# Optimization experiments

Measured on AMD Instinct MI355X. Metric: run time of the kernel, lower is better.

Reference implementation:

```python
import jax, jax.numpy as jnp
import numpy as np

# FP4 e2m1 lookup: nibble -> value (bit3 = sign, bits2:0 = e2m1 magnitude)
FP4_LUT = jnp.array([0.0, 0.5, 1.0, 1.5, 2.0, 3.0, 4.0, 6.0,
                     -0.0, -0.5, -1.0, -1.5, -2.0, -3.0, -4.0, -6.0], dtype=jnp.float32)
BLOCK = 16  # elements per micro-scale (one uint8 E8M0 scale per 16 fp4 values)


def _dequant(packed, sf):
    """packed: [R, K//2] int bytes (two fp4 nibbles each, low nibble first).
    sf: [R, K//16] E8M0 exponents (value = 2^(sf-127)). Returns [R, K] f32."""
    R, Kh = packed.shape
    K = Kh * 2
    lo = packed & 0xF
    hi = (packed >> 4) & 0xF
    nib = jnp.stack([lo, hi], axis=-1).reshape(R, K)
    vals = FP4_LUT[nib]  # [R, K]
    block_scale = jnp.exp2((sf - 127).astype(jnp.float32))  # [R, K//16]
    return (vals.reshape(R, K // BLOCK, BLOCK) * block_scale[:, :, None]).reshape(R, K)


def setup_inputs() -> dict:
    key = jax.random.key(0)
    ks = jax.random.split(key, 6)
    M, N, K = 8192, 4096, 4224  # K = in_features(4096) + select_num(128)
    A_packed = jax.random.randint(ks[0], (M, K // 2), 0, 256, dtype=jnp.int32)
    SFA = jax.random.randint(ks[1], (M, K // BLOCK), 118, 134, dtype=jnp.int32)
    B_packed = jax.random.randint(ks[2], (N, K // 2), 0, 256, dtype=jnp.int32)
    SFB = jax.random.randint(ks[3], (N, K // BLOCK), 118, 134, dtype=jnp.int32)
    scale = jax.random.uniform(ks[4], (1,), dtype=jnp.float32, minval=0.5, maxval=1.5)
    bias = jax.random.normal(ks[5], (N,), dtype=jnp.float32)
    return {"A_packed": A_packed, "SFA": SFA, "scale": scale,
            "B_packed": B_packed, "SFB": SFB, "bias": bias}


def reference(A_packed, SFA, scale, B_packed, SFB, bias):
    A = _dequant(A_packed, SFA)        # [M, K]
    B = _dequant(B_packed, SFB)        # [N, K]
    # y = scale * (A @ B^T) + bias   (self.scale == 1.0 folded into scale)
    y = scale[0] * jnp.einsum('mk,nk->mn', A, B) + bias[None, :]
    return y
```

## Files before the change

### kernel.cpp

```cpp
#include <hip/hip_runtime.h>
#include <stdint.h>

#define M_DIM 8192
#define N_DIM 4096
#define K_DIM 4224
#define BK 64

typedef float f32x16 __attribute__((ext_vector_type(16)));
typedef int   i32x8  __attribute__((ext_vector_type(8)));
typedef int   i32x4  __attribute__((ext_vector_type(4)));

#define RAW_BARRIER()  asm volatile("s_barrier" ::: "memory")
#define WAIT_VM4()     asm volatile("s_waitcnt vmcnt(4)" ::: "memory")
#define WAIT_VM0()     asm volatile("s_waitcnt vmcnt(0)" ::: "memory")

__device__ __forceinline__ uint32_t conv4(uint32_t x, uint32_t k1) {
    uint32_t n7   = x & 0x07070707u;
    uint32_t base = __builtin_amdgcn_perm(0x46444240u, 0x3E3C3800u, n7);
    uint32_t nz   = __builtin_amdgcn_perm(0x01010101u, 0x01010100u, n7);
    uint32_t sign = (x & 0x08080808u) << 4;
    return (base + nz * k1 - (nz << 6)) | sign;
}

__global__ __launch_bounds__(256) void dequant_all(
    const int* __restrict__ Ap, const int* __restrict__ SFA, uint8_t* __restrict__ Aout,
    const int* __restrict__ Bp, const int* __restrict__ SFB, uint8_t* __restrict__ Bout)
{
    const int nhA = M_DIM * K_DIM / 32;
    int i = blockIdx.x * 256 + threadIdx.x;
    const int* p; const int* sf; uint8_t* out; int idx;
    if (i < nhA) { p = Ap; sf = SFA; out = Aout; idx = i; }
    else         { p = Bp; sf = SFB; out = Bout; idx = i - nhA; }

    const int4* p4 = (const int4*)p;
    int4 q0 = p4[4 * idx];
    int4 q1 = p4[4 * idx + 1];
    int4 q2 = p4[4 * idx + 2];
    int4 q3 = p4[4 * idx + 3];
    int2 sfp = ((const int2*)sf)[idx];
    uint32_t k1a = (uint32_t)(((sfp.x - 127) << 2) + 64);
    uint32_t k1b = (uint32_t)(((sfp.y - 127) << 2) + 64);

    uint32_t o[8];
#pragma unroll
    for (int g = 0; g < 4; ++g) {
        int4 pg = (g == 0) ? q0 : (g == 1) ? q1 : (g == 2) ? q2 : q3;
        uint32_t k1 = (g < 2) ? k1a : k1b;
        uint32_t w = (uint32_t)(pg.x & 0xFF) | ((uint32_t)(pg.y & 0xFF) << 8) |
                     ((uint32_t)(pg.z & 0xFF) << 16) | ((uint32_t)pg.w << 24);
        uint32_t lr = conv4(w & 0x0F0F0F0Fu, k1);
        uint32_t hr = conv4((w >> 4) & 0x0F0F0F0Fu, k1);
        o[2 * g]     = __builtin_amdgcn_perm(hr, lr, 0x05010400u);
        o[2 * g + 1] = __builtin_amdgcn_perm(hr, lr, 0x07030602u);
    }
    *(uint4*)(out + (size_t)idx * 32)      = make_uint4(o[0], o[1], o[2], o[3]);
    *(uint4*)(out + (size_t)idx * 32 + 16) = make_uint4(o[4], o[5], o[6], o[7]);
}

__global__ __launch_bounds__(512, 2) void gemm_mx(
    const uint8_t* __restrict__ A, const uint8_t* __restrict__ B,
    const float* __restrict__ scale, const float* __restrict__ bias,
    float* __restrict__ C)
{
    __shared__ uint8_t smem[131072];

    const int tid  = threadIdx.x;
    const int lane = tid & 63;
    const int w    = tid >> 6;
    const int wm   = w >> 2;
    const int wn   = w & 3;
    const int r31  = lane & 31;
    const int h    = lane >> 5;

    const int lin = blockIdx.y * 16 + blockIdx.x;
    const int o   = (lin & 7) * 64 + (lin >> 3);
    const int bn0 = (o & 15) * 256;
    const int bm0 = (o >> 4) * 256;

    f32x16 acc[4][2];
#pragma unroll
    for (int i = 0; i < 4; ++i)
#pragma unroll
        for (int j = 0; j < 2; ++j)
            acc[i][j] = (f32x16)(0.0f);

    const int srow = lane >> 2;
    const int scol = (((lane & 3) ^ ((lane >> 3) & 3)) << 4);
    const uint8_t* Ag = A + (size_t)(bm0 + w * 32 + srow) * K_DIM + scol;
    const uint8_t* Bg = B + (size_t)(bn0 + w * 32 + srow) * K_DIM + scol;
    uint8_t* Asw = smem + w * 2048;
    uint8_t* Bsw = smem + 16384 + w * 2048;

#define STAGE(koff, boff)                                                        \
    do {                                                                         \
        const uint8_t* ag_ = Ag + (koff);                                        \
        const uint8_t* bg_ = Bg + (koff);                                        \
        __builtin_amdgcn_global_load_lds(                                        \
            (const __attribute__((address_space(1))) void*)(ag_),                \
            (__attribute__((address_space(3))) void*)(Asw + (boff)), 16, 0, 0);  \
        __builtin_amdgcn_global_load_lds(                                        \
            (const __attribute__((address_space(1))) void*)(ag_ + (size_t)16 * K_DIM), \
            (__attribute__((address_space(3))) void*)(Asw + (boff) + 1024), 16, 0, 0); \
        __builtin_amdgcn_global_load_lds(                                        \
            (const __attribute__((address_space(1))) void*)(bg_),                \
            (__attribute__((address_space(3))) void*)(Bsw + (boff)), 16, 0, 0);  \
        __builtin_amdgcn_global_load_lds(                                        \
            (const __attribute__((address_space(1))) void*)(bg_ + (size_t)16 * K_DIM), \
            (__attribute__((address_space(3))) void*)(Bsw + (boff) + 1024), 16, 0, 0); \
    } while (0)

    const int sx = (r31 >> 1) & 3;
    const uint8_t* pa_lo[4]; const uint8_t* pa_hi[4];
    const uint8_t* pb_lo[2]; const uint8_t* pb_hi[2];
#pragma unroll
    for (int mi = 0; mi < 4; ++mi) {
        const uint8_t* base = smem + (wm * 128 + mi * 32 + r31) * 64;
        pa_lo[mi] = base + (((2 * h)     ^ sx) << 4);
        pa_hi[mi] = base + (((2 * h + 1) ^ sx) << 4);
    }
#pragma unroll
    for (int ni = 0; ni < 2; ++ni) {
        const uint8_t* base = smem + 16384 + (wn * 64 + ni * 32 + r31) * 64;
        pb_lo[ni] = base + (((2 * h)     ^ sx) << 4);
        pb_hi[ni] = base + (((2 * h + 1) ^ sx) << 4);
    }

    i32x8 afX0[2], afX1[2], bfX0[2], bfX1[2], afY[2];

    auto rd = [&](const uint8_t* plo, const uint8_t* phi, int off, i32x8& dst) {
        i32x4 lo = *(const i32x4*)(plo + off);
        i32x4 hi = *(const i32x4*)(phi + off);
        dst = __builtin_shufflevector(lo, hi, 0, 1, 2, 3, 4, 5, 6, 7);
    };
    auto mm = [&](const i32x8& a, const i32x8& b, f32x16& c) {
        c = __builtin_amdgcn_mfma_scale_f32_32x32x64_f8f6f4(
                a, b, c, 1, 1, 0, 0x7F7F7F7F, 0, 0x7F7F7F7F);
    };

#define CORE(AC, BC, AN, BN, OBN)                             \
    __builtin_amdgcn_s_setprio(1);                            \
    mm(AC[0], BC[0], acc[0][0]); mm(AC[0], BC[1], acc[0][1]); \
    mm(AC[1], BC[0], acc[1][0]); mm(AC[1], BC[1], acc[1][1]); \
    __builtin_amdgcn_s_setprio(0);                            \
    rd(pa_lo[0], pa_hi[0], OBN, AN[0]);                       \
    rd(pa_lo[1], pa_hi[1], OBN, AN[1]);                       \
    rd(pb_lo[0], pb_hi[0], OBN, BN[0]);                       \
    rd(pb_lo[1], pb_hi[1], OBN, BN[1]);                       \
    __builtin_amdgcn_s_setprio(1);                            \
    mm(afY[0], BC[0], acc[2][0]); mm(afY[0], BC[1], acc[2][1]); \
    mm(afY[1], BC[0], acc[3][0]); mm(afY[1], BC[1], acc[3][1]); \
    __builtin_amdgcn_s_setprio(0);                            \
    rd(pa_lo[2], pa_hi[2], OBN, afY[0]);                      \
    rd(pa_lo[3], pa_hi[3], OBN, afY[1]);

#define BODY(T, AC, BC, AN, BN, OBN, OBS)                     \
    STAGE(((T) + 3) * BK, OBS);                               \
    CORE(AC, BC, AN, BN, OBN)                                 \
    WAIT_VM4(); RAW_BARRIER();

    STAGE(0 * BK, 0);
    STAGE(1 * BK, 32768);
    STAGE(2 * BK, 65536);
    WAIT_VM4();
    RAW_BARRIER();
    rd(pa_lo[0], pa_hi[0], 0, afX0[0]);
    rd(pa_lo[1], pa_hi[1], 0, afX0[1]);
    rd(pb_lo[0], pb_hi[0], 0, bfX0[0]);
    rd(pb_lo[1], pb_hi[1], 0, bfX0[1]);
    rd(pa_lo[2], pa_hi[2], 0, afY[0]);
    rd(pa_lo[3], pa_hi[3], 0, afY[1]);

#pragma unroll 1
    for (int g = 0; g < 15; ++g) {
        const int t = 4 * g;
        BODY(t,     afX0, bfX0, afX1, bfX1, 32768, 98304)
        BODY(t + 1, afX1, bfX1, afX0, bfX0, 65536, 0)
        BODY(t + 2, afX0, bfX0, afX1, bfX1, 98304, 32768)
        BODY(t + 3, afX1, bfX1, afX0, bfX0, 0,     65536)
    }
    BODY(60, afX0, bfX0, afX1, bfX1, 32768, 98304)
    BODY(61, afX1, bfX1, afX0, bfX0, 65536, 0)
    BODY(62, afX0, bfX0, afX1, bfX1, 98304, 32768)
    CORE(afX1, bfX1, afX0, bfX0, 0)
    WAIT_VM0(); RAW_BARRIER();
    CORE(afX0, bfX0, afX1, bfX1, 32768)
    __builtin_amdgcn_s_setprio(1);
    mm(afX1[0], bfX1[0], acc[0][0]); mm(afX1[0], bfX1[1], acc[0][1]);
    mm(afX1[1], bfX1[0], acc[1][0]); mm(afX1[1], bfX1[1], acc[1][1]);
    mm(afY[0],  bfX1[0], acc[2][0]); mm(afY[0],  bfX1[1], acc[2][1]);
    mm(afY[1],  bfX1[0], acc[3][0]); mm(afY[1],  bfX1[1], acc[3][1]);
    __builtin_amdgcn_s_setprio(0);
#undef BODY
#undef CORE
#undef STAGE

    const float sc = scale[0];
#pragma unroll
    for (int ni = 0; ni < 2; ++ni) {
        const int col = bn0 + wn * 64 + ni * 32 + r31;
        const float bv = bias[col];
#pragma unroll
        for (int mi = 0; mi < 4; ++mi) {
            const int rbase = bm0 + wm * 128 + mi * 32 + 4 * h;
#pragma unroll
            for (int reg = 0; reg < 16; ++reg) {
                const int row = rbase + (reg & 3) + 8 * (reg >> 2);
                C[(size_t)row * N_DIM + col] = sc * acc[mi][ni][reg] + bv;
            }
        }
    }
}

extern "C" void kernel_launch(void* const* d_in, const int* in_sizes, int n_in,
                              void* d_out, int out_size, void* d_ws, size_t ws_size,
                              hipStream_t stream) {
    const int*   A_packed = (const int*)d_in[0];
    const int*   SFA      = (const int*)d_in[1];
    const float* scale    = (const float*)d_in[2];
    const int*   B_packed = (const int*)d_in[3];
    const int*   SFB      = (const int*)d_in[4];
    const float* bias     = (const float*)d_in[5];
    float*       out      = (float*)d_out;

    uint8_t* Abf8 = (uint8_t*)d_ws;
    uint8_t* Bbf8 = Abf8 + (size_t)M_DIM * K_DIM;

    const int npairA = M_DIM * K_DIM / 32;
    const int npairB = N_DIM * K_DIM / 32;
    dequant_all<<<(npairA + npairB) / 256, 256, 0, stream>>>(
        A_packed, SFA, Abf8, B_packed, SFB, Bbf8);

    dim3 grid(N_DIM / 256, M_DIM / 256);
    gemm_mx<<<grid, 512, 0, stream>>>(Abf8, Bbf8, scale, bias, out);
}
```

Before: 340.4 us.

## Use 4 waves per block with 128x128 warp tiles in MX GEMM

Halves the threads per block from 512 to 256. Each wave now computes a 128x128 output tile (4x4 MFMA accumulators) instead of 128x64, so fragment reuse per LDS read goes up and per-wave LDS traffic per MFMA goes down. Each wave now issues 8 global-to-LDS loads per stage, and the wait count is raised to match. The cost is much higher register pressure (256 accumulator VGPRs plus doubled fragments) and fewer waves per CU to hide latency, with occupancy limited to one block.

```diff
diff --git a/kernel.cpp b/kernel.cpp
--- a/kernel.cpp
+++ b/kernel.cpp
@@ -11,7 +11,7 @@
 typedef int   i32x4  __attribute__((ext_vector_type(4)));
 
 #define RAW_BARRIER()  asm volatile("s_barrier" ::: "memory")
-#define WAIT_VM4()     asm volatile("s_waitcnt vmcnt(4)" ::: "memory")
+#define WAIT_VM8()     asm volatile("s_waitcnt vmcnt(8)" ::: "memory")
 #define WAIT_VM0()     asm volatile("s_waitcnt vmcnt(0)" ::: "memory")
 
 __device__ __forceinline__ uint32_t conv4(uint32_t x, uint32_t k1) {
@@ -57,7 +57,7 @@
     *(uint4*)(out + (size_t)idx * 32 + 16) = make_uint4(o[4], o[5], o[6], o[7]);
 }
 
-__global__ __launch_bounds__(512, 2) void gemm_mx(
+__global__ __launch_bounds__(256, 1) void gemm_mx(
     const uint8_t* __restrict__ A, const uint8_t* __restrict__ B,
     const float* __restrict__ scale, const float* __restrict__ bias,
     float* __restrict__ C)
@@ -67,8 +67,8 @@
     const int tid  = threadIdx.x;
     const int lane = tid & 63;
     const int w    = tid >> 6;
-    const int wm   = w >> 2;
-    const int wn   = w & 3;
+    const int wm   = w >> 1;
+    const int wn   = w & 1;
     const int r31  = lane & 31;
     const int h    = lane >> 5;
 
@@ -77,41 +77,42 @@
     const int bn0 = (o & 15) * 256;
     const int bm0 = (o >> 4) * 256;
 
-    f32x16 acc[4][2];
+    f32x16 acc[4][4];
 #pragma unroll
     for (int i = 0; i < 4; ++i)
 #pragma unroll
-        for (int j = 0; j < 2; ++j)
+        for (int j = 0; j < 4; ++j)
             acc[i][j] = (f32x16)(0.0f);
 
     const int srow = lane >> 2;
     const int scol = (((lane & 3) ^ ((lane >> 3) & 3)) << 4);
-    const uint8_t* Ag = A + (size_t)(bm0 + w * 32 + srow) * K_DIM + scol;
-    const uint8_t* Bg = B + (size_t)(bn0 + w * 32 + srow) * K_DIM + scol;
-    uint8_t* Asw = smem + w * 2048;
-    uint8_t* Bsw = smem + 16384 + w * 2048;
+    const uint8_t* Ag = A + (size_t)(bm0 + w * 64 + srow) * K_DIM + scol;
+    const uint8_t* Bg = B + (size_t)(bn0 + w * 64 + srow) * K_DIM + scol;
+    uint8_t* Asw = smem + w * 4096;
+    uint8_t* Bsw = smem + 16384 + w * 4096;
+
+#define GLDS(gp, lp)                                                             \
+    __builtin_amdgcn_global_load_lds(                                            \
+        (const __attribute__((address_space(1))) void*)(gp),                     \
+        (__attribute__((address_space(3))) void*)(lp), 16, 0, 0)
 
 #define STAGE(koff, boff)                                                        \
     do {                                                                         \
         const uint8_t* ag_ = Ag + (koff);                                        \
         const uint8_t* bg_ = Bg + (koff);                                        \
-        __builtin_amdgcn_global_load_lds(                                        \
-            (const __attribute__((address_space(1))) void*)(ag_),                \
-            (__attribute__((address_space(3))) void*)(Asw + (boff)), 16, 0, 0);  \
-        __builtin_amdgcn_global_load_lds(                                        \
-            (const __attribute__((address_space(1))) void*)(ag_ + (size_t)16 * K_DIM), \
-            (__attribute__((address_space(3))) void*)(Asw + (boff) + 1024), 16, 0, 0); \
-        __builtin_amdgcn_global_load_lds(                                        \
-            (const __attribute__((address_space(1))) void*)(bg_),                \
-            (__attribute__((address_space(3))) void*)(Bsw + (boff)), 16, 0, 0);  \
-        __builtin_amdgcn_global_load_lds(                                        \
-            (const __attribute__((address_space(1))) void*)(bg_ + (size_t)16 * K_DIM), \
-            (__attribute__((address_space(3))) void*)(Bsw + (boff) + 1024), 16, 0, 0); \
+        GLDS(ag_,                       Asw + (boff));                           \
+        GLDS(ag_ + (size_t)16 * K_DIM,  Asw + (boff) + 1024);                    \
+        GLDS(ag_ + (size_t)32 * K_DIM,  Asw + (boff) + 2048);                    \
+        GLDS(ag_ + (size_t)48 * K_DIM,  Asw + (boff) + 3072);                    \
+        GLDS(bg_,                       Bsw + (boff));                           \
+        GLDS(bg_ + (size_t)16 * K_DIM,  Bsw + (boff) + 1024);                    \
+        GLDS(bg_ + (size_t)32 * K_DIM,  Bsw + (boff) + 2048);                    \
+        GLDS(bg_ + (size_t)48 * K_DIM,  Bsw + (boff) + 3072);                    \
     } while (0)
 
     const int sx = (r31 >> 1) & 3;
     const uint8_t* pa_lo[4]; const uint8_t* pa_hi[4];
-    const uint8_t* pb_lo[2]; const uint8_t* pb_hi[2];
+    const uint8_t* pb_lo[4]; const uint8_t* pb_hi[4];
 #pragma unroll
     for (int mi = 0; mi < 4; ++mi) {
         const uint8_t* base = smem + (wm * 128 + mi * 32 + r31) * 64;
@@ -119,13 +120,13 @@
         pa_hi[mi] = base + (((2 * h + 1) ^ sx) << 4);
     }
 #pragma unroll
-    for (int ni = 0; ni < 2; ++ni) {
-        const uint8_t* base = smem + 16384 + (wn * 64 + ni * 32 + r31) * 64;
+    for (int ni = 0; ni < 4; ++ni) {
+        const uint8_t* base = smem + 16384 + (wn * 128 + ni * 32 + r31) * 64;
         pb_lo[ni] = base + (((2 * h)     ^ sx) << 4);
         pb_hi[ni] = base + (((2 * h + 1) ^ sx) << 4);
     }
 
-    i32x8 afX0[2], afX1[2], bfX0[2], bfX1[2], afY[2];
+    i32x8 afX0[4], afX1[4], bfX0[4], bfX1[4];
 
     auto rd = [&](const uint8_t* plo, const uint8_t* phi, int off, i32x8& dst) {
         i32x4 lo = *(const i32x4*)(plo + off);
@@ -137,46 +138,51 @@
                 a, b, c, 1, 1, 0, 0x7F7F7F7F, 0, 0x7F7F7F7F);
     };
 
+#define CLUSTER(AC, BC, MI)                                   \
+    __builtin_amdgcn_s_setprio(1);                            \
+    mm(AC[MI], BC[0], acc[MI][0]); mm(AC[MI], BC[1], acc[MI][1]); \
+    mm(AC[MI], BC[2], acc[MI][2]); mm(AC[MI], BC[3], acc[MI][3]); \
+    __builtin_amdgcn_s_setprio(0);
+
 #define CORE(AC, BC, AN, BN, OBN)                             \
-    __builtin_amdgcn_s_setprio(1);                            \
-    mm(AC[0], BC[0], acc[0][0]); mm(AC[0], BC[1], acc[0][1]); \
-    mm(AC[1], BC[0], acc[1][0]); mm(AC[1], BC[1], acc[1][1]); \
-    __builtin_amdgcn_s_setprio(0);                            \
+    CLUSTER(AC, BC, 0)                                        \
     rd(pa_lo[0], pa_hi[0], OBN, AN[0]);                       \
+    rd(pb_lo[0], pb_hi[0], OBN, BN[0]);                       \
+    CLUSTER(AC, BC, 1)                                        \
     rd(pa_lo[1], pa_hi[1], OBN, AN[1]);                       \
-    rd(pb_lo[0], pb_hi[0], OBN, BN[0]);                       \
     rd(pb_lo[1], pb_hi[1], OBN, BN[1]);                       \
-    __builtin_amdgcn_s_setprio(1);                            \
-    mm(afY[0], BC[0], acc[2][0]); mm(afY[0], BC[1], acc[2][1]); \
-    mm(afY[1], BC[0], acc[3][0]); mm(afY[1], BC[1], acc[3][1]); \
-    __builtin_amdgcn_s_setprio(0);                            \
-    rd(pa_lo[2], pa_hi[2], OBN, afY[0]);                      \
-    rd(pa_lo[3], pa_hi[3], OBN, afY[1]);
+    CLUSTER(AC, BC, 2)                                        \
+    rd(pa_lo[2], pa_hi[2], OBN, AN[2]);                       \
+    rd(pb_lo[2], pb_hi[2], OBN, BN[2]);                       \
+    CLUSTER(AC, BC, 3)                                        \
+    rd(pa_lo[3], pa_hi[3], OBN, AN[3]);                       \
+    rd(pb_lo[3], pb_hi[3], OBN, BN[3]);
 
 #define BODY(T, AC, BC, AN, BN, OBN, OBS)                     \
     STAGE(((T) + 3) * BK, OBS);                               \
     CORE(AC, BC, AN, BN, OBN)                                 \
-    WAIT_VM4(); RAW_BARRIER();
+    WAIT_VM8(); RAW_BARRIER();
 
     STAGE(0 * BK, 0);
     STAGE(1 * BK, 32768);
     STAGE(2 * BK, 65536);
-    WAIT_VM4();
+    WAIT_VM8();
     RAW_BARRIER();
     rd(pa_lo[0], pa_hi[0], 0, afX0[0]);
     rd(pa_lo[1], pa_hi[1], 0, afX0[1]);
+    rd(pa_lo[2], pa_hi[2], 0, afX0[2]);
+    rd(pa_lo[3], pa_hi[3], 0, afX0[3]);
     rd(pb_lo[0], pb_hi[0], 0, bfX0[0]);
     rd(pb_lo[1], pb_hi[1], 0, bfX0[1]);
-    rd(pa_lo[2], pa_hi[2], 0, afY[0]);
-    rd(pa_lo[3], pa_hi[3], 0, afY[1]);
+    rd(pb_lo[2], pb_hi[2], 0, bfX0[2]);
+    rd(pb_lo[3], pb_hi[3], 0, bfX0[3]);
 
 #pragma unroll 1
     for (int g = 0; g < 15; ++g) {
-        const int t = 4 * g;
-        BODY(t,     afX0, bfX0, afX1, bfX1, 32768, 98304)
-        BODY(t + 1, afX1, bfX1, afX0, bfX0, 65536, 0)
-        BODY(t + 2, afX0, bfX0, afX1, bfX1, 98304, 32768)
-        BODY(t + 3, afX1, bfX1, afX0, bfX0, 0,     65536)
+        BODY(4 * g,     afX0, bfX0, afX1, bfX1, 32768, 98304)
+        BODY(4 * g + 1, afX1, bfX1, afX0, bfX0, 65536, 0)
+        BODY(4 * g + 2, afX0, bfX0, afX1, bfX1, 98304, 32768)
+        BODY(4 * g + 3, afX1, bfX1, afX0, bfX0, 0,     65536)
     }
     BODY(60, afX0, bfX0, afX1, bfX1, 32768, 98304)
     BODY(61, afX1, bfX1, afX0, bfX0, 65536, 0)
@@ -184,20 +190,20 @@
     CORE(afX1, bfX1, afX0, bfX0, 0)
     WAIT_VM0(); RAW_BARRIER();
     CORE(afX0, bfX0, afX1, bfX1, 32768)
-    __builtin_amdgcn_s_setprio(1);
-    mm(afX1[0], bfX1[0], acc[0][0]); mm(afX1[0], bfX1[1], acc[0][1]);
-    mm(afX1[1], bfX1[0], acc[1][0]); mm(afX1[1], bfX1[1], acc[1][1]);
-    mm(afY[0],  bfX1[0], acc[2][0]); mm(afY[0],  bfX1[1], acc[2][1]);
-    mm(afY[1],  bfX1[0], acc[3][0]); mm(afY[1],  bfX1[1], acc[3][1]);
-    __builtin_amdgcn_s_setprio(0);
+    CLUSTER(afX1, bfX1, 0)
+    CLUSTER(afX1, bfX1, 1)
+    CLUSTER(afX1, bfX1, 2)
+    CLUSTER(afX1, bfX1, 3)
 #undef BODY
 #undef CORE
+#undef CLUSTER
 #undef STAGE
+#undef GLDS
 
     const float sc = scale[0];
 #pragma unroll
-    for (int ni = 0; ni < 2; ++ni) {
-        const int col = bn0 + wn * 64 + ni * 32 + r31;
+    for (int ni = 0; ni < 4; ++ni) {
+        const int col = bn0 + wn * 128 + ni * 32 + r31;
         const float bv = bias[col];
 #pragma unroll
         for (int mi = 0; mi < 4; ++mi) {
@@ -231,5 +237,5 @@
         A_packed, SFA, Abf8, B_packed, SFB, Bbf8);
 
     dim3 grid(N_DIM / 256, M_DIM / 256);
-    gemm_mx<<<grid, 512, 0, stream>>>(Abf8, Bbf8, scale, bias, out);
-}
+    gemm_mx<<<grid, 256, 0, stream>>>(Abf8, Bbf8, scale, bias, out);
+}
```

After: 336.8 us. Within noise of the previous version (-1.1%).
